# Performance work log

Hardware: AMD Instinct MI355X
Metric: run time of the kernel (lower is better)

Reference implementation:

```python
import jax, jax.numpy as jnp
import numpy as np

N_TOTAL, N_IDS, S, K, D = 100000, 20000, 8, 16, 128
H_VC, H_EC = 9, D // 4

def setup_inputs() -> dict:
    key = jax.random.key(0)
    ks = jax.random.split(key, 8)
    return {
        "ids": jax.random.randint(ks[0], (N_IDS,), 0, N_TOTAL),
        "feats": jax.random.normal(ks[1], (N_TOTAL, D), dtype=jnp.float32),
        "adj": jax.random.randint(ks[2], (N_TOTAL, S, K), 0, N_TOTAL),
        "vc_w1": jax.random.normal(ks[3], (D, H_VC), dtype=jnp.float32) * (1.0 / np.sqrt(D)),
        "vc_b1": jnp.zeros((H_VC,), jnp.float32),
        "vc_w2": jax.random.normal(ks[4], (H_VC, 1), dtype=jnp.float32) * (1.0 / np.sqrt(H_VC)),
        "vc_b2": jnp.zeros((1,), jnp.float32),
        "ec_w1": jax.random.normal(ks[5], (D, H_EC), dtype=jnp.float32) * (1.0 / np.sqrt(D)),
        "ec_b1": jnp.zeros((H_EC,), jnp.float32),
        "ec_w2": jax.random.normal(ks[6], (H_EC, 1), dtype=jnp.float32) * (1.0 / np.sqrt(H_EC)),
        "ec_b2": jnp.zeros((1,), jnp.float32),
        "fc_w": jax.random.normal(ks[7], (D, D), dtype=jnp.float32) * (1.0 / np.sqrt(D)),
        "fc_b": jnp.zeros((D,), jnp.float32),
    }

def edge_conv(x, w1, b1, w2, b2):
    # x: (..., t, d); attention-pooled mean over axis -2 -> (..., d)
    h = jax.nn.relu(x @ w1 + b1)          # (..., t, hidden)
    scores = h @ w2 + b2                   # (..., t, 1)
    scores = jax.nn.softmax(scores, axis=-2)
    return jnp.sum(scores * x, axis=-2)

def reference(ids, feats, adj, vc_w1, vc_b1, vc_w2, vc_b2,
              ec_w1, ec_b1, ec_w2, ec_b2, fc_w, fc_b):
    a = adj[ids]                           # (N, s, k) hyperedge member indices
    g = feats[a]                           # (N, s, k, d) irregular gather
    # vertex conv: pool k members of each hyperedge -> (N, s, d)
    he = edge_conv(g, vc_w1, vc_b1, vc_w2, vc_b2)
    # edge conv: pool s hyperedges per vertex -> (N, d)
    x = edge_conv(he, ec_w1, ec_b1, ec_w2, ec_b2)
    # dropout is identity at eval; activation = relu
    return jax.nn.relu(x @ fc_w + fc_b)
```

## Files before the change

kernel.cpp:

```cpp
#include <hip/hip_runtime.h>


constexpr int S_   = 8;
constexpr int K_   = 16;
constexpr int D_   = 128;
constexpr int HVC  = 9;
constexpr int HEC  = 32;

__device__ __forceinline__ float rl_f(float v, int lane) {
    return __int_as_float(__builtin_amdgcn_readlane(__float_as_int(v), lane));
}

__global__ __launch_bounds__(256)
void dhg_score1(const float* __restrict__ feats,
                const float* __restrict__ vc_w1, const float* __restrict__ vc_b1,
                const float* __restrict__ vc_w2, const float* __restrict__ vc_b2,
                float* __restrict__ score1, int n_total)
{
    const int n = blockIdx.x * 256 + threadIdx.x;
    if (n >= n_total) return;
    const float* rp = feats + (size_t)n * D_;

    float h[HVC];
    #pragma unroll
    for (int j = 0; j < HVC; ++j) h[j] = vc_b1[j];

    #pragma unroll 4
    for (int i = 0; i < D_ / 4; ++i) {
        const float4 gv = *(const float4*)(rp + 4 * i);
        const float gc[4] = {gv.x, gv.y, gv.z, gv.w};
        #pragma unroll
        for (int c = 0; c < 4; ++c) {
            #pragma unroll
            for (int j = 0; j < HVC; ++j)
                h[j] = fmaf(gc[c], vc_w1[(4 * i + c) * HVC + j], h[j]);
        }
    }
    float sc = vc_b2[0];
    #pragma unroll
    for (int j = 0; j < HVC; ++j) sc = fmaf(fmaxf(h[j], 0.0f), vc_w2[j], sc);
    score1[n] = sc;
}

__device__ __forceinline__ float softmax16(float sc) {
    float mx = sc;
    #pragma unroll
    for (int m = 1; m <= 8; m <<= 1) mx = fmaxf(mx, __shfl_xor(mx, m));
    const float e = __expf(sc - mx);
    float z = e;
    #pragma unroll
    for (int m = 1; m <= 8; m <<= 1) z += __shfl_xor(z, m);
    return e / z;
}

__global__ __launch_bounds__(128, 4)
void dhg_main(const int* __restrict__ ids,
              const float* __restrict__ feats,
              const int* __restrict__ adj,
              const float* __restrict__ score1,
              const float* __restrict__ ec_w1, const float* __restrict__ ec_b1,
              const float* __restrict__ ec_w2, const float* __restrict__ ec_b2,
              const float* __restrict__ fc_w,  const float* __restrict__ fc_b,
              float* __restrict__ out, int n_ids)
{
    __shared__ float he_lds[2][S_ * 129];
    __shared__ float x_lds[2][D_];

    const int wave = threadIdx.x >> 6;
    const int lane = threadIdx.x & 63;
    int wid = blockIdx.x * 2 + wave;
    if (wid >= n_ids) wid = n_ids - 1;

    const int node = ids[wid];
    const int* arow = adj + (size_t)(unsigned)node * (S_ * K_);
    const int miA = arow[lane];
    const int miB = arow[lane + 64];

    const float wA = softmax16(score1[miA]);
    const float wB = softmax16(score1[miB]);

    float he_lo[S_], he_hi[S_];

    #pragma unroll
    for (int g = 0; g < 2; ++g) {
        const int   mi = g ? miB : miA;
        const float w  = g ? wB  : wA;
        #pragma unroll
        for (int sl = 0; sl < 4; ++sl) {
            const int s = g * 4 + sl;
            float2 fv[K_];
            #pragma unroll
            for (int k = 0; k < K_; ++k) {
                const int mik = __builtin_amdgcn_readlane(mi, sl * 16 + k);
                fv[k] = *(const float2*)(feats + (size_t)(unsigned)mik * D_ + 2 * lane);
            }
            float alo = 0.0f, ahi = 0.0f;
            #pragma unroll
            for (int k = 0; k < K_; ++k) {
                const float wk = rl_f(w, sl * 16 + k);
                alo = fmaf(wk, fv[k].x, alo);
                ahi = fmaf(wk, fv[k].y, ahi);
            }
            he_lo[s] = alo;
            he_hi[s] = ahi;
            he_lds[wave][s * 129 + 2 * lane]     = alo;
            he_lds[wave][s * 129 + 2 * lane + 1] = ahi;
        }
    }

    __builtin_amdgcn_wave_barrier();

    const int s8 = lane & 7;
    const int jg = lane >> 3;
    const float* hrow = &he_lds[wave][s8 * 129];
    float a0 = 0.0f, a1 = 0.0f, a2 = 0.0f, a3 = 0.0f;
    #pragma unroll 4
    for (int d = 0; d < D_; ++d) {
        const float hv = hrow[d];
        const float4 wv = *(const float4*)(ec_w1 + d * HEC + 4 * jg);
        a0 = fmaf(hv, wv.x, a0);
        a1 = fmaf(hv, wv.y, a1);
        a2 = fmaf(hv, wv.z, a2);
        a3 = fmaf(hv, wv.w, a3);
    }
    const float4 b4  = *(const float4*)(ec_b1 + 4 * jg);
    const float4 w24 = *(const float4*)(ec_w2 + 4 * jg);
    float p = 0.0f;
    p = fmaf(fmaxf(a0 + b4.x, 0.0f), w24.x, p);
    p = fmaf(fmaxf(a1 + b4.y, 0.0f), w24.y, p);
    p = fmaf(fmaxf(a2 + b4.z, 0.0f), w24.z, p);
    p = fmaf(fmaxf(a3 + b4.w, 0.0f), w24.w, p);
    #pragma unroll
    for (int m = 8; m <= 32; m <<= 1) p += __shfl_xor(p, m);
    const float sc2 = p + ec_b2[0];

    float mx2 = sc2;
    #pragma unroll
    for (int m = 1; m <= 4; m <<= 1) mx2 = fmaxf(mx2, __shfl_xor(mx2, m));
    const float e2 = __expf(sc2 - mx2);
    float z2 = e2;
    #pragma unroll
    for (int m = 1; m <= 4; m <<= 1) z2 += __shfl_xor(z2, m);
    const float p2 = e2 / z2;

    float x_lo = 0.0f, x_hi = 0.0f;
    #pragma unroll
    for (int s = 0; s < S_; ++s) {
        const float ps = rl_f(p2, s);
        x_lo = fmaf(ps, he_lo[s], x_lo);
        x_hi = fmaf(ps, he_hi[s], x_hi);
    }
    x_lds[wave][2 * lane]     = x_lo;
    x_lds[wave][2 * lane + 1] = x_hi;

    __builtin_amdgcn_wave_barrier();

    const float* xr = x_lds[wave];
    float2 acc = *(const float2*)(fc_b + 2 * lane);
    #pragma unroll 8
    for (int d = 0; d < D_; ++d) {
        const float xv = xr[d];
        const float2 wv = *(const float2*)(fc_w + d * D_ + 2 * lane);
        acc.x = fmaf(xv, wv.x, acc.x);
        acc.y = fmaf(xv, wv.y, acc.y);
    }
    float2 o;
    o.x = fmaxf(acc.x, 0.0f);
    o.y = fmaxf(acc.y, 0.0f);
    *(float2*)(out + (size_t)(unsigned)wid * D_ + 2 * lane) = o;
}

extern "C" void kernel_launch(void* const* d_in, const int* in_sizes, int n_in,
                              void* d_out, int out_size, void* d_ws, size_t ws_size,
                              hipStream_t stream)
{
    const int*   ids   = (const int*)d_in[0];
    const float* feats = (const float*)d_in[1];
    const int*   adj   = (const int*)d_in[2];
    const float* vc_w1 = (const float*)d_in[3];
    const float* vc_b1 = (const float*)d_in[4];
    const float* vc_w2 = (const float*)d_in[5];
    const float* vc_b2 = (const float*)d_in[6];
    const float* ec_w1 = (const float*)d_in[7];
    const float* ec_b1 = (const float*)d_in[8];
    const float* ec_w2 = (const float*)d_in[9];
    const float* ec_b2 = (const float*)d_in[10];
    const float* fc_w  = (const float*)d_in[11];
    const float* fc_b  = (const float*)d_in[12];
    float* out = (float*)d_out;

    const int n_ids   = in_sizes[0];
    const int n_total = in_sizes[1] / D_;
    float* score1 = (float*)d_ws;

    dhg_score1<<<(n_total + 255) / 256, 256, 0, stream>>>(
        feats, vc_w1, vc_b1, vc_w2, vc_b2, score1, n_total);

    const int blocks = (n_ids + 1) / 2;
    dhg_main<<<blocks, 128, 0, stream>>>(ids, feats, adj, score1,
                                         ec_w1, ec_b1, ec_w2, ec_b2,
                                         fc_w, fc_b, out, n_ids);
}
```

Baseline: 385.2 us.

## Gather half-precision feature copy in main kernel; wave-per-row score kernel

The score kernel now assigns one wave per feature row, does the 128x9 dot products with cross-lane reductions, and also writes an fp16 copy of all features into workspace. The main kernel, when workspace is large enough, gathers 16-member hyperedge features from the fp16 copy, halving the bytes of the random 2.56M-row gather. The cost is an extra full write of a 25.6MB fp16 table each call and reduced precision of the pooled features.

```diff
diff --git a/kernel.cpp b/kernel.cpp
--- a/kernel.cpp
+++ b/kernel.cpp
@@ -1,4 +1,5 @@
 #include <hip/hip_runtime.h>
+#include <hip/hip_fp16.h>
 
 
 constexpr int S_   = 8;
@@ -15,31 +16,32 @@
 void dhg_score1(const float* __restrict__ feats,
                 const float* __restrict__ vc_w1, const float* __restrict__ vc_b1,
                 const float* __restrict__ vc_w2, const float* __restrict__ vc_b2,
-                float* __restrict__ score1, int n_total)
+                float* __restrict__ score1, __half2* __restrict__ feats_h,
+                int n_total)
 {
-    const int n = blockIdx.x * 256 + threadIdx.x;
+    const int wave = threadIdx.x >> 6;
+    const int lane = threadIdx.x & 63;
+    const int n = blockIdx.x * 4 + wave;
     if (n >= n_total) return;
-    const float* rp = feats + (size_t)n * D_;
-
+
+    const float2 v = *(const float2*)(feats + (size_t)n * D_ + 2 * lane);
+    if (feats_h) feats_h[(size_t)n * 64 + lane] = __float22half2_rn(v);
+
+    const float* wp = vc_w1 + (2 * lane) * HVC;
     float h[HVC];
     #pragma unroll
-    for (int j = 0; j < HVC; ++j) h[j] = vc_b1[j];
-
-    #pragma unroll 4
-    for (int i = 0; i < D_ / 4; ++i) {
-        const float4 gv = *(const float4*)(rp + 4 * i);
-        const float gc[4] = {gv.x, gv.y, gv.z, gv.w};
+    for (int j = 0; j < HVC; ++j) h[j] = fmaf(v.x, wp[j], v.y * wp[HVC + j]);
+
+    #pragma unroll
+    for (int j = 0; j < HVC; ++j) {
         #pragma unroll
-        for (int c = 0; c < 4; ++c) {
-            #pragma unroll
-            for (int j = 0; j < HVC; ++j)
-                h[j] = fmaf(gc[c], vc_w1[(4 * i + c) * HVC + j], h[j]);
-        }
+        for (int m = 1; m <= 32; m <<= 1) h[j] += __shfl_xor(h[j], m);
     }
     float sc = vc_b2[0];
     #pragma unroll
-    for (int j = 0; j < HVC; ++j) sc = fmaf(fmaxf(h[j], 0.0f), vc_w2[j], sc);
-    score1[n] = sc;
+    for (int j = 0; j < HVC; ++j)
+        sc = fmaf(fmaxf(h[j] + vc_b1[j], 0.0f), vc_w2[j], sc);
+    if (lane == 0) score1[n] = sc;
 }
 
 __device__ __forceinline__ float softmax16(float sc) {
@@ -53,9 +55,11 @@
     return e / z;
 }
 
+template<bool HALF>
 __global__ __launch_bounds__(128, 4)
 void dhg_main(const int* __restrict__ ids,
               const float* __restrict__ feats,
+              const __half2* __restrict__ feats_h,
               const int* __restrict__ adj,
               const float* __restrict__ score1,
               const float* __restrict__ ec_w1, const float* __restrict__ ec_b1,
@@ -88,18 +92,34 @@
         #pragma unroll
         for (int sl = 0; sl < 4; ++sl) {
             const int s = g * 4 + sl;
-            float2 fv[K_];
-            #pragma unroll
-            for (int k = 0; k < K_; ++k) {
-                const int mik = __builtin_amdgcn_readlane(mi, sl * 16 + k);
-                fv[k] = *(const float2*)(feats + (size_t)(unsigned)mik * D_ + 2 * lane);
-            }
             float alo = 0.0f, ahi = 0.0f;
-            #pragma unroll
-            for (int k = 0; k < K_; ++k) {
-                const float wk = rl_f(w, sl * 16 + k);
-                alo = fmaf(wk, fv[k].x, alo);
-                ahi = fmaf(wk, fv[k].y, ahi);
+            if constexpr (HALF) {
+                __half2 fv[K_];
+                #pragma unroll
+                for (int k = 0; k < K_; ++k) {
+                    const int mik = __builtin_amdgcn_readlane(mi, sl * 16 + k);
+                    fv[k] = feats_h[(size_t)(unsigned)mik * 64 + lane];
+                }
+                #pragma unroll
+                for (int k = 0; k < K_; ++k) {
+                    const float wk = rl_f(w, sl * 16 + k);
+                    const float2 f = __half22float2(fv[k]);
+                    alo = fmaf(wk, f.x, alo);
+                    ahi = fmaf(wk, f.y, ahi);
+                }
+            } else {
+                float2 fv[K_];
+                #pragma unroll
+                for (int k = 0; k < K_; ++k) {
+                    const int mik = __builtin_amdgcn_readlane(mi, sl * 16 + k);
+                    fv[k] = *(const float2*)(feats + (size_t)(unsigned)mik * D_ + 2 * lane);
+                }
+                #pragma unroll
+                for (int k = 0; k < K_; ++k) {
+                    const float wk = rl_f(w, sl * 16 + k);
+                    alo = fmaf(wk, fv[k].x, alo);
+                    ahi = fmaf(wk, fv[k].y, ahi);
+                }
             }
             he_lo[s] = alo;
             he_hi[s] = ahi;
@@ -191,13 +211,22 @@
 
     const int n_ids   = in_sizes[0];
     const int n_total = in_sizes[1] / D_;
+
     float* score1 = (float*)d_ws;
-
-    dhg_score1<<<(n_total + 255) / 256, 256, 0, stream>>>(
-        feats, vc_w1, vc_b1, vc_w2, vc_b2, score1, n_total);
+    const size_t half_off = 512 * 1024;
+    const size_t need = half_off + (size_t)n_total * 64 * sizeof(__half2);
+    __half2* feats_h = (ws_size >= need) ? (__half2*)((char*)d_ws + half_off) : nullptr;
+
+    dhg_score1<<<(n_total + 3) / 4, 256, 0, stream>>>(
+        feats, vc_w1, vc_b1, vc_w2, vc_b2, score1, feats_h, n_total);
 
     const int blocks = (n_ids + 1) / 2;
-    dhg_main<<<blocks, 128, 0, stream>>>(ids, feats, adj, score1,
-                                         ec_w1, ec_b1, ec_w2, ec_b2,
-                                         fc_w, fc_b, out, n_ids);
-}
+    if (feats_h)
+        dhg_main<true><<<blocks, 128, 0, stream>>>(ids, feats, feats_h, adj, score1,
+                                                   ec_w1, ec_b1, ec_w2, ec_b2,
+                                                   fc_w, fc_b, out, n_ids);
+    else
+        dhg_main<false><<<blocks, 128, 0, stream>>>(ids, feats, nullptr, adj, score1,
+                                                    ec_w1, ec_b1, ec_w2, ec_b2,
+                                                    fc_w, fc_b, out, n_ids);
+}
```

Result: faster. 370.0 us (-3.9%).
